# Kernel optimization log

Measured on AMD Instinct MI355X. Metric: run time of the kernel, lower is better.

## Reference

```python
import jax, jax.numpy as jnp
import numpy as np


def setup_inputs() -> dict:
    key = jax.random.key(0)
    k1, k2, k3, k4 = jax.random.split(key, 4)
    B, D, N, M = 4, 256, 4096, 4096
    return {
        "src": jax.random.normal(k1, (B, 3, N), dtype=jnp.float32),
        "tgt": jax.random.normal(k2, (B, 3, M), dtype=jnp.float32),
        "src_emb": jax.random.normal(k3, (B, D, N), dtype=jnp.float32),
        "tgt_emb": jax.random.normal(k4, (B, D, M), dtype=jnp.float32),
    }


def reference(src, tgt, src_emb, tgt_emb):
    # pairwise_distance[b,n,m] = -||src_emb[:,n] - tgt_emb[:,m]||^2
    # decomposed as -xx + 2*inner - yy (inner below is -2*dot, as in torch code)
    inner = -2.0 * jnp.einsum("bdn,bdm->bnm", src_emb, tgt_emb)       # [B,N,M]
    xx = jnp.sum(src_emb ** 2, axis=1)[:, :, None]                     # [B,N,1]
    yy = jnp.sum(tgt_emb ** 2, axis=1)[:, None, :]                     # [B,1,M]
    pairwise_distance = -xx - inner - yy                               # [B,N,M]
    scores = jax.nn.softmax(pairwise_distance, axis=2)                 # softmax over tgt points
    # src_corr[b,c,n] = sum_m tgt[b,c,m] * scores[b,n,m]
    src_corr = jnp.einsum("bcm,bnm->bcn", tgt, scores)                 # [B,3,N]
    return src_corr
```

## Files before the change

kernel.cpp:

```cpp
#include <hip/hip_runtime.h>

#define NBATCH 4
#define DDIM   256
#define NN     4096
#define MM     4096
#define NCHUNK 8
#define MCHUNK 512
#define MTILE  32
#define LOG2E  1.44269504088896340736f

using half8   = __attribute__((ext_vector_type(8))) _Float16;
using floatx4 = __attribute__((ext_vector_type(4))) float;


__global__ __launch_bounds__(256) void k_prep(const float* __restrict__ src_emb,
                                              const float* __restrict__ tgt_emb,
                                              const float* __restrict__ tgt,
                                              _Float16* __restrict__ Qf,
                                              _Float16* __restrict__ Kf,
                                              float* __restrict__ yyS,
                                              float4* __restrict__ Vt) {
    __shared__ __align__(16) float tile[128 * 64];
    __shared__ float psum[4][64];
    int i = blockIdx.x;
    int tensor = i & 1, b = (i >> 1) & 3, dg = (i >> 3) & 1, ng = i >> 4;
    int t = threadIdx.x, w = t >> 6, lane = t & 63;
    const float* in = tensor ? tgt_emb : src_emb;
    _Float16* outp  = tensor ? Kf : Qf;
    const float scale = tensor ? 1.0f : 2.0f * LOG2E;

    const char* gb = (const char*)(in + ((size_t)b * DDIM + dg * 128 + w * 32) * NN + ng * 64);
    char* lb = (char*)tile + w * 8192;
#pragma unroll
    for (int it = 0; it < 8; it++) {
        __builtin_amdgcn_global_load_lds(
            (const __attribute__((address_space(1))) uint32_t*)(const void*)
                (gb + (size_t)(it * 4 + (lane >> 4)) * (NN * 4) + (lane & 15) * 16),
            (__attribute__((address_space(3))) uint32_t*)(void*)
                (lb + it * 1024),
            16, 0, 0);
    }
    __syncthreads();

    float ss = 0.f;
    half8* ob = (half8*)(outp + (size_t)b * NN * DDIM);
    int n_glob = ng * 64 + lane;
    int blk = n_glob >> 4, l15 = n_glob & 15;
#pragma unroll
    for (int q = 0; q < 4; q++) {
        int octg = w * 4 + q;
        half8 v;
#pragma unroll
        for (int k = 0; k < 8; k++) {
            float f = tile[(octg * 8 + k) * 64 + lane];
            ss = fmaf(f, f, ss);
            v[k] = (_Float16)(f * scale);
        }
        int dglob = dg * 128 + octg * 8;
        int dsg = dglob >> 5, oct = (dglob >> 3) & 3;
        ob[(((size_t)blk * 8 + dsg) * 4 + oct) * 16 + l15] = v;
    }
    if (tensor) {
        psum[w][lane] = ss;
        __syncthreads();
        if (t < 64) {
            float s = (psum[0][t] + psum[1][t]) + (psum[2][t] + psum[3][t]);
            s *= -LOG2E;
            int m = ng * 64 + t;
            if (dg == 0) {
                const float* tp = tgt + (size_t)b * 3 * MM + m;
                Vt[(size_t)b * MM + m] = make_float4(tp[0], tp[MM], tp[2 * MM], s);
            } else {
                yyS[(size_t)b * MM + m] = s;
            }
        }
    }
}

__global__ __launch_bounds__(256, 2) void k_flash(const _Float16* __restrict__ Qf,
                                                  const _Float16* __restrict__ Kf,
                                                  const float* __restrict__ yyS,
                                                  const float4* __restrict__ Vt,
                                                  float4* __restrict__ Opart,
                                                  float* __restrict__ Mpart) {
    __shared__ __align__(16) _Float16 Kt[2][MTILE * DDIM];
    __shared__ floatx4 vtt[MCHUNK];

    int i = blockIdx.x, t = threadIdx.x;
    int xcd = i & 7, j = i >> 3;
    int b = xcd >> 1, nhalf = xcd & 1;
    int chunk = j & 7, ntile = nhalf * 16 + (j >> 3);

    int wave = t >> 6, lane = t & 63, quad = lane >> 4, l15 = lane & 15;
    int m0 = chunk * MCHUNK;
    int mblk0 = m0 >> 4;

    const char* kfb = (const char*)(Kf + (size_t)b * NN * DDIM);
    auto stage = [&](int mt) {
        const char* gb = kfb + (size_t)(mblk0 + mt * 2) * 8192 + wave * 4096;
        char* lb = (char*)&Kt[mt & 1][0] + wave * 4096;
#pragma unroll
        for (int it = 0; it < 4; it++) {
            __builtin_amdgcn_global_load_lds(
                (const __attribute__((address_space(1))) uint32_t*)(const void*)
                    (gb + it * 1024 + lane * 16),
                (__attribute__((address_space(3))) uint32_t*)(void*)
                    (lb + it * 1024),
                16, 0, 0);
        }
    };

    stage(0);

    {
        const float4* vb = Vt + (size_t)b * MM + m0;
        const float* yb = yyS + (size_t)b * MM + m0;
        for (int r = t; r < MCHUNK; r += 256) {
            float4 g = vb[r];
            vtt[r] = (floatx4){g.x, g.y, g.z, g.w + yb[r]};
        }
    }

    int nblk0 = ntile * 8 + wave * 2;
    const half8* qp = (const half8*)Qf + (size_t)b * NN * 32;
    half8 qf[2][8];
#pragma unroll
    for (int nb = 0; nb < 2; nb++)
#pragma unroll
        for (int ds = 0; ds < 8; ds++)
            qf[nb][ds] = qp[(((size_t)(nblk0 + nb) * 8 + ds) * 4 + quad) * 16 + l15];

    const floatx4 z4 = {0.f, 0.f, 0.f, 0.f};
    floatx4 o[2] = {z4, z4};
    float mr[2] = {-__builtin_inff(), -__builtin_inff()};

    for (int mt = 0; mt < MCHUNK / MTILE; mt++) {
        __syncthreads();
        if (mt + 1 < MCHUNK / MTILE) stage(mt + 1);

        const char* Kb = (const char*)&Kt[mt & 1][0];
        floatx4 acc[2][2] = {{z4, z4}, {z4, z4}};
        __builtin_amdgcn_s_setprio(1);
#pragma unroll
        for (int mb = 0; mb < 2; mb++) {
            const char* rb = Kb + mb * 8192 + lane * 16;
#pragma unroll
            for (int ds = 0; ds < 8; ds++) {
                half8 a = *(const half8*)(rb + ds * 1024);
                acc[mb][0] = __builtin_amdgcn_mfma_f32_16x16x32_f16(a, qf[0][ds], acc[mb][0], 0, 0, 0);
                acc[mb][1] = __builtin_amdgcn_mfma_f32_16x16x32_f16(a, qf[1][ds], acc[mb][1], 0, 0, 0);
            }
        }
        __builtin_amdgcn_s_setprio(0);

        int vbase = mt * MTILE;
        float yv[8];
#pragma unroll
        for (int r = 0; r < 4; r++) {
            yv[r]     = ((const float*)&vtt[vbase + quad * 4 + r])[3];
            yv[4 + r] = ((const float*)&vtt[vbase + 16 + quad * 4 + r])[3];
        }
#pragma unroll
        for (int nb = 0; nb < 2; nb++) {
#pragma unroll
            for (int r = 0; r < 4; r++) {
                acc[0][nb][r] += yv[r];
                acc[1][nb][r] += yv[4 + r];
            }
            float tm = fmaxf(fmaxf(fmaxf(acc[0][nb][0], acc[0][nb][1]),
                                   fmaxf(acc[0][nb][2], acc[0][nb][3])),
                             fmaxf(fmaxf(acc[1][nb][0], acc[1][nb][1]),
                                   fmaxf(acc[1][nb][2], acc[1][nb][3])));
            float mn = fmaxf(mr[nb], tm);
            float al = __builtin_amdgcn_exp2f(mr[nb] - mn);
            mr[nb] = mn;
            o[nb] = o[nb] * al;
        }
#pragma unroll
        for (int jj = 0; jj < 8; jj++) {
            floatx4 vr = vtt[vbase + (jj >> 2) * 16 + quad * 4 + (jj & 3)];
#pragma unroll
            for (int nb = 0; nb < 2; nb++) {
                float p = __builtin_amdgcn_exp2f(acc[jj >> 2][nb][jj & 3] - mr[nb]);
                o[nb][0] = fmaf(p, vr[0], o[nb][0]);
                o[nb][1] = fmaf(p, vr[1], o[nb][1]);
                o[nb][2] = fmaf(p, vr[2], o[nb][2]);
                o[nb][3] += p;
            }
        }
    }

#pragma unroll
    for (int nb = 0; nb < 2; nb++) {
        float mq = mr[nb];
        float ma = fmaxf(mq, __shfl_xor(mq, 16, 64));
        ma = fmaxf(ma, __shfl_xor(ma, 32, 64));
        float wgt = __builtin_amdgcn_exp2f(mq - ma);
        floatx4 ow = o[nb] * wgt;
#pragma unroll
        for (int c = 0; c < 4; c++) {
            float v = ow[c];
            v += __shfl_xor(v, 16, 64);
            v += __shfl_xor(v, 32, 64);
            ow[c] = v;
        }
        if (quad == 0) {
            int n = (nblk0 + nb) * 16 + l15;
            size_t idx = (size_t)(chunk * NBATCH + b) * NN + n;
            Opart[idx] = make_float4(ow[0], ow[1], ow[2], ow[3]);
            Mpart[idx] = ma;
        }
    }
}

__global__ __launch_bounds__(128) void k_combine(const float4* __restrict__ Opart,
                                                 const float* __restrict__ Mpart,
                                                 float* __restrict__ out) {
    int idx = blockIdx.x * 128 + threadIdx.x;
    int b = idx >> 12, n = idx & (NN - 1);
    float mstar = -__builtin_inff();
#pragma unroll
    for (int j = 0; j < NCHUNK; j++)
        mstar = fmaxf(mstar, Mpart[(size_t)(j * NBATCH + b) * NN + n]);
    float o0 = 0.f, o1 = 0.f, o2 = 0.f, l = 0.f;
#pragma unroll
    for (int j = 0; j < NCHUNK; j++) {
        size_t id = (size_t)(j * NBATCH + b) * NN + n;
        float w = __builtin_amdgcn_exp2f(Mpart[id] - mstar);
        float4 P = Opart[id];
        o0 = fmaf(w, P.x, o0); o1 = fmaf(w, P.y, o1);
        o2 = fmaf(w, P.z, o2); l  = fmaf(w, P.w, l);
    }
    out[(size_t)(b * 3 + 0) * NN + n] = o0 / l;
    out[(size_t)(b * 3 + 1) * NN + n] = o1 / l;
    out[(size_t)(b * 3 + 2) * NN + n] = o2 / l;
}

extern "C" void kernel_launch(void* const* d_in, const int* in_sizes, int n_in,
                              void* d_out, int out_size, void* d_ws, size_t ws_size,
                              hipStream_t stream) {
    const float* tgt     = (const float*)d_in[1];
    const float* src_emb = (const float*)d_in[2];
    const float* tgt_emb = (const float*)d_in[3];
    float* out = (float*)d_out;

    char* ws = (char*)d_ws;
    _Float16* Qf  = (_Float16*)(ws);
    _Float16* Kf  = (_Float16*)(ws + 8388608);
    float*    yyS = (float*)   (ws + 16777216);
    float4*   Vt  = (float4*)  (ws + 16842752);
    float4*   Op  = (float4*)  (ws + 17104896);
    float*    Mp  = (float*)   (ws + 19202048);

    hipLaunchKernelGGL(k_prep,    dim3(1024), dim3(256), 0, stream,
                       src_emb, tgt_emb, tgt, Qf, Kf, yyS, Vt);
    hipLaunchKernelGGL(k_flash,   dim3(1024), dim3(256), 0, stream, Qf, Kf, yyS, Vt, Op, Mp);
    hipLaunchKernelGGL(k_combine, dim3(128),  dim3(128), 0, stream, Op, Mp, out);
}
```

Baseline: 134.0 us.

## Prefetch K tiles with explicit waitcnt barriers and store V as fp16 in LDS

Replaces the per-iteration __syncthreads with hand-placed s_barrier and s_waitcnt vmcnt sequences. Tile 1 is now staged before the loop and each iteration stages tile mt+2 into the buffer it just freed, so global-to-LDS copies overlap compute without a full memory drain at every barrier. Separately, the tgt coordinates are packed into an fp16 half4 LDS array, and the yy term moves to its own float array. This shrinks LDS traffic for the V reads, at the cost of reduced precision in the weighted coordinate sums and a more fragile manual synchronization scheme.

```diff
diff --git a/kernel.cpp b/kernel.cpp
--- a/kernel.cpp
+++ b/kernel.cpp
@@ -9,6 +9,7 @@
 #define MTILE  32
 #define LOG2E  1.44269504088896340736f
 
+using half4   = __attribute__((ext_vector_type(4))) _Float16;
 using half8   = __attribute__((ext_vector_type(8))) _Float16;
 using floatx4 = __attribute__((ext_vector_type(4))) float;
 
@@ -84,7 +85,8 @@
                                                   float4* __restrict__ Opart,
                                                   float* __restrict__ Mpart) {
     __shared__ __align__(16) _Float16 Kt[2][MTILE * DDIM];
-    __shared__ floatx4 vtt[MCHUNK];
+    __shared__ __align__(8)  half4 vh[MCHUNK];
+    __shared__ float yyt[MCHUNK];
 
     int i = blockIdx.x, t = threadIdx.x;
     int xcd = i & 7, j = i >> 3;
@@ -106,7 +108,7 @@
                     (gb + it * 1024 + lane * 16),
                 (__attribute__((address_space(3))) uint32_t*)(void*)
                     (lb + it * 1024),
-                16, 0, 0);
+            16, 0, 0);
         }
     };
 
@@ -117,7 +119,10 @@
         const float* yb = yyS + (size_t)b * MM + m0;
         for (int r = t; r < MCHUNK; r += 256) {
             float4 g = vb[r];
-            vtt[r] = (floatx4){g.x, g.y, g.z, g.w + yb[r]};
+            half4 h; h[0] = (_Float16)g.x; h[1] = (_Float16)g.y;
+            h[2] = (_Float16)g.z; h[3] = (_Float16)0.f;
+            vh[r] = h;
+            yyt[r] = g.w + yb[r];
         }
     }
 
@@ -130,14 +135,16 @@
         for (int ds = 0; ds < 8; ds++)
             qf[nb][ds] = qp[(((size_t)(nblk0 + nb) * 8 + ds) * 4 + quad) * 16 + l15];
 
+    stage(1);
+
+    asm volatile("s_waitcnt vmcnt(4)" ::: "memory");
+    asm volatile("s_barrier" ::: "memory");
+
     const floatx4 z4 = {0.f, 0.f, 0.f, 0.f};
     floatx4 o[2] = {z4, z4};
     float mr[2] = {-__builtin_inff(), -__builtin_inff()};
 
     for (int mt = 0; mt < MCHUNK / MTILE; mt++) {
-        __syncthreads();
-        if (mt + 1 < MCHUNK / MTILE) stage(mt + 1);
-
         const char* Kb = (const char*)&Kt[mt & 1][0];
         floatx4 acc[2][2] = {{z4, z4}, {z4, z4}};
         __builtin_amdgcn_s_setprio(1);
@@ -157,8 +164,8 @@
         float yv[8];
 #pragma unroll
         for (int r = 0; r < 4; r++) {
-            yv[r]     = ((const float*)&vtt[vbase + quad * 4 + r])[3];
-            yv[4 + r] = ((const float*)&vtt[vbase + 16 + quad * 4 + r])[3];
+            yv[r]     = yyt[vbase + quad * 4 + r];
+            yv[4 + r] = yyt[vbase + 16 + quad * 4 + r];
         }
 #pragma unroll
         for (int nb = 0; nb < 2; nb++) {
@@ -178,15 +185,27 @@
         }
 #pragma unroll
         for (int jj = 0; jj < 8; jj++) {
-            floatx4 vr = vtt[vbase + (jj >> 2) * 16 + quad * 4 + (jj & 3)];
+            half4 vrh = vh[vbase + (jj >> 2) * 16 + quad * 4 + (jj & 3)];
+            float v0 = (float)vrh[0], v1 = (float)vrh[1], v2 = (float)vrh[2];
 #pragma unroll
             for (int nb = 0; nb < 2; nb++) {
                 float p = __builtin_amdgcn_exp2f(acc[jj >> 2][nb][jj & 3] - mr[nb]);
-                o[nb][0] = fmaf(p, vr[0], o[nb][0]);
-                o[nb][1] = fmaf(p, vr[1], o[nb][1]);
-                o[nb][2] = fmaf(p, vr[2], o[nb][2]);
+                o[nb][0] = fmaf(p, v0, o[nb][0]);
+                o[nb][1] = fmaf(p, v1, o[nb][1]);
+                o[nb][2] = fmaf(p, v2, o[nb][2]);
                 o[nb][3] += p;
             }
+        }
+
+        if (mt < MCHUNK / MTILE - 1) {
+            asm volatile("s_barrier" ::: "memory");
+            if (mt + 2 < MCHUNK / MTILE) {
+                stage(mt + 2);
+                asm volatile("s_waitcnt vmcnt(4)" ::: "memory");
+            } else {
+                asm volatile("s_waitcnt vmcnt(0)" ::: "memory");
+            }
+            asm volatile("s_barrier" ::: "memory");
         }
     }
 
```

Result: faster. 127.7 us (-4.7%).
